# Kernel optimization log

Hardware: AMD Instinct MI355X
Metric: run time of the kernel (lower is better)

The kernel has to match this reference:

```python
import jax, jax.numpy as jnp
import numpy as np

N, E, B = 8000, 128000, 16
DIN, D, H, C, L = 16, 256, 8, 32, 6
MC, NT = 200, 8
NEG_SLOPE = 0.2


def layernorm(x, s, b):
    mu = jnp.mean(x, axis=-1, keepdims=True)
    var = jnp.mean(jnp.square(x - mu), axis=-1, keepdims=True)
    return (x - mu) * jax.lax.rsqrt(var + 1e-5) * s + b


def setup_inputs() -> dict:
    key = jax.random.key(0)
    ks = iter(jax.random.split(key, 64))
    rn = lambda shape, s=0.05: jax.random.normal(next(ks), shape, jnp.float32) * s
    inp = {}
    inp['x'] = jax.random.normal(next(ks), (N, DIN), jnp.float32)
    inp['edge_index'] = jax.random.randint(next(ks), (2, E), 0, N)
    inp['batch'] = jnp.sort(jax.random.randint(next(ks), (N,), 0, B))
    # node encoder: Linear(DIN,D) + LayerNorm
    inp['enc_W'] = rn((DIN, D)); inp['enc_b'] = jnp.zeros((D,), jnp.float32)
    inp['enc_ls'] = jnp.ones((D,), jnp.float32); inp['enc_lb'] = jnp.zeros((D,), jnp.float32)
    # GATv2 layers (stacked): lin_l, lin_r, att, output bias, post LayerNorm
    inp['Wl'] = rn((L, D, D)); inp['bl'] = jnp.zeros((L, D), jnp.float32)
    inp['Wr'] = rn((L, D, D)); inp['br'] = jnp.zeros((L, D), jnp.float32)
    inp['att'] = rn((L, H, C))
    inp['gb'] = jnp.zeros((L, D), jnp.float32)
    inp['gls'] = jnp.ones((L, D), jnp.float32); inp['glb'] = jnp.zeros((L, D), jnp.float32)
    # color head MLP: D -> D -> D//2 -> MC
    inp['cW1'] = rn((D, D)); inp['cb1'] = jnp.zeros((D,), jnp.float32)
    inp['cW2'] = rn((D, D // 2)); inp['cb2'] = jnp.zeros((D // 2,), jnp.float32)
    inp['cW3'] = rn((D // 2, MC)); inp['cb3'] = jnp.zeros((MC,), jnp.float32)
    # chromatic head: 2D -> D -> D//2 -> MC
    inp['chW1'] = rn((2 * D, D)); inp['chb1'] = jnp.zeros((D,), jnp.float32)
    inp['chW2'] = rn((D, D // 2)); inp['chb2'] = jnp.zeros((D // 2,), jnp.float32)
    inp['chW3'] = rn((D // 2, MC)); inp['chb3'] = jnp.zeros((MC,), jnp.float32)
    # type head: 2D -> 128 -> NT
    inp['tW1'] = rn((2 * D, 128)); inp['tb1'] = jnp.zeros((128,), jnp.float32)
    inp['tW2'] = rn((128, NT)); inp['tb2'] = jnp.zeros((NT,), jnp.float32)
    # difficulty head: 2D -> 64 -> 1, sigmoid * 100
    inp['dW1'] = rn((2 * D, 64)); inp['db1'] = jnp.zeros((64,), jnp.float32)
    inp['dW2'] = rn((64, 1)); inp['db2'] = jnp.zeros((1,), jnp.float32)
    return inp


def reference(x, edge_index, batch, enc_W, enc_b, enc_ls, enc_lb,
              Wl, bl, Wr, br, att, gb, gls, glb,
              cW1, cb1, cW2, cb2, cW3, cb3,
              chW1, chb1, chW2, chb2, chW3, chb3,
              tW1, tb1, tW2, tb2, dW1, db1, dW2, db2):
    n = x.shape[0]
    # node encoder (dropout = identity at inference)
    h = jax.nn.relu(layernorm(x @ enc_W + enc_b, enc_ls, enc_lb))
    # add self loops once (same for every layer)
    sl = jnp.arange(n)
    src = jnp.concatenate([edge_index[0], sl])  # message source j
    dst = jnp.concatenate([edge_index[1], sl])  # message target i
    for i in range(L):
        xl = (h @ Wl[i] + bl[i]).reshape(n, H, C)  # source transform
        xr = (h @ Wr[i] + br[i]).reshape(n, H, C)  # target transform
        # GATv2 attention: a^T LeakyReLU(xl_j + xr_i)
        e = jax.nn.leaky_relu(xl[src] + xr[dst], NEG_SLOPE)  # [E+N, H, C]
        logits = jnp.einsum('ehc,hc->eh', e, att[i])          # [E+N, H]
        # segment softmax over destination node (self-loops guarantee denom > 0)
        m = jax.ops.segment_max(logits, dst, num_segments=n)
        m = jnp.where(jnp.isfinite(m), m, 0.0)
        p = jnp.exp(logits - m[dst])
        denom = jax.ops.segment_sum(p, dst, num_segments=n)
        alpha = p / denom[dst]
        out = jax.ops.segment_sum(xl[src] * alpha[:, :, None], dst, num_segments=n)
        out = out.reshape(n, D) + gb[i]
        h_new = jax.nn.elu(layernorm(out, gls[i], glb[i]))
        h = h + h_new if i > 0 else h_new
    # per-node color logits
    z = jax.nn.relu(h @ cW1 + cb1)
    z = jax.nn.relu(z @ cW2 + cb2)
    node_colors = z @ cW3 + cb3
    # global mean/max pooling per graph
    cnt = jax.ops.segment_sum(jnp.ones((n,), h.dtype), batch, num_segments=B)
    mean_p = jax.ops.segment_sum(h, batch, num_segments=B) / jnp.maximum(cnt, 1.0)[:, None]
    max_p = jax.ops.segment_max(h, batch, num_segments=B)
    max_p = jnp.where(jnp.isfinite(max_p), max_p, 0.0)
    g = jnp.concatenate([mean_p, max_p], axis=1)  # [B, 2D]
    zc = jax.nn.relu(g @ chW1 + chb1)
    zc = jax.nn.relu(zc @ chW2 + chb2)
    chromatic_num = zc @ chW3 + chb3
    zt = jax.nn.relu(g @ tW1 + tb1)
    graph_type = zt @ tW2 + tb2
    zd = jax.nn.relu(g @ dW1 + db1)
    difficulty = jax.nn.sigmoid(zd @ dW2 + db2) * 100.0
    return (node_colors, chromatic_num, graph_type, difficulty)
```

## Files before the change

### kernel.cpp

```cpp
#include <hip/hip_runtime.h>
#include <hip/hip_bf16.h>

constexpr int DIN = 16;
constexpr int D   = 256;
constexpr int NH  = 8;
constexpr int NC  = 32;
constexpr int MC  = 200;
constexpr int NT  = 8;
constexpr int BG  = 16;
constexpr int NL  = 6;
constexpr int PS  = 16;
constexpr float NEG = 0.2f;

typedef __attribute__((ext_vector_type(8))) short bfrag;
typedef __attribute__((ext_vector_type(4))) float f32x4;

__device__ inline unsigned short f2bf(float f) {
    unsigned int u = __float_as_uint(f);
    u += 0x7FFFu + ((u >> 16) & 1u);
    return (unsigned short)(u >> 16);
}
__device__ inline float bf2f(unsigned short u) {
    return __uint_as_float((unsigned int)u << 16);
}

__device__ inline float dot_ilp(const float* g, const float* __restrict__ W, int K, int ldw, int t) {
    float a0 = 0.f, a1 = 0.f, a2 = 0.f, a3 = 0.f;
    for (int k = 0; k < K; k += 4) {
        a0 = fmaf(g[k + 0], W[(k + 0) * ldw + t], a0);
        a1 = fmaf(g[k + 1], W[(k + 1) * ldw + t], a1);
        a2 = fmaf(g[k + 2], W[(k + 2) * ldw + t], a2);
        a3 = fmaf(g[k + 3], W[(k + 3) * ldw + t], a3);
    }
    return (a0 + a1) + (a2 + a3);
}


__device__ inline void enc_node(const float* x, const float* W, const float* b, const float* ls,
                                const float* lb, float* h, int n, int lane) {
    int c4 = lane * 4;
    float xs[DIN];
#pragma unroll
    for (int k = 0; k < DIN; k += 4) {
        float4 xv = *(const float4*)&x[n * DIN + k];
        xs[k] = xv.x; xs[k + 1] = xv.y; xs[k + 2] = xv.z; xs[k + 3] = xv.w;
    }
    float4 a = *(const float4*)&b[c4];
#pragma unroll
    for (int k = 0; k < DIN; k++) {
        float4 wv = *(const float4*)&W[k * D + c4];
        a.x = fmaf(xs[k], wv.x, a.x);
        a.y = fmaf(xs[k], wv.y, a.y);
        a.z = fmaf(xs[k], wv.z, a.z);
        a.w = fmaf(xs[k], wv.w, a.w);
    }
    float s = a.x + a.y + a.z + a.w;
#pragma unroll
    for (int msk = 1; msk <= 32; msk <<= 1) s += __shfl_xor(s, msk);
    float mu = s * (1.f / D);
    float4 dv = make_float4(a.x - mu, a.y - mu, a.z - mu, a.w - mu);
    float v2 = dv.x * dv.x + dv.y * dv.y + dv.z * dv.z + dv.w * dv.w;
#pragma unroll
    for (int msk = 1; msk <= 32; msk <<= 1) v2 += __shfl_xor(v2, msk);
    float rstd = rsqrtf(v2 * (1.f / D) + 1e-5f);
    float4 lsv = *(const float4*)&ls[c4];
    float4 lbv = *(const float4*)&lb[c4];
    float4 y = make_float4(fmaxf(dv.x * rstd * lsv.x + lbv.x, 0.f),
                           fmaxf(dv.y * rstd * lsv.y + lbv.y, 0.f),
                           fmaxf(dv.z * rstd * lsv.z + lbv.z, 0.f),
                           fmaxf(dv.w * rstd * lsv.w + lbv.w, 0.f));
    *(float4*)&h[(size_t)n * D + c4] = y;
}

__device__ inline float4 attn_compute(const unsigned short* xl, const unsigned short* xr,
                                      const int* row_ptr, const int* col, const float* att,
                                      const float* gb, const float* gls, const float* glb,
                                      const float* h, int layer, int n, int lane) {
    int c4 = lane * 4;
    ushort4 xr4 = *(const ushort4*)&xr[(size_t)n * D + c4];
    float4 xrv = make_float4(bf2f(xr4.x), bf2f(xr4.y), bf2f(xr4.z), bf2f(xr4.w));
    float4 av  = *(const float4*)&att[c4];
    int beg = row_ptr[n], end = row_ptr[n + 1];
    int deg = end - beg;
    int myc = col[beg + min(lane, deg - 1)];
    float l = 0.f;
    float4 acc = make_float4(0.f, 0.f, 0.f, 0.f);
    auto loadx = [&](int i) -> ushort4 {
        if (i < deg) {
            int s = (i < 64) ? __shfl(myc, i) : col[beg + i];
            return *(const ushort4*)&xl[(size_t)s * D + c4];
        }
        return make_ushort4(0, 0, 0, 0);
    };
    auto step = [&](ushort4 x4) {
        float4 xlv = make_float4(bf2f(x4.x), bf2f(x4.y), bf2f(x4.z), bf2f(x4.w));
        float sx = xlv.x + xrv.x; sx = sx > 0.f ? sx : NEG * sx;
        float sy = xlv.y + xrv.y; sy = sy > 0.f ? sy : NEG * sy;
        float sz = xlv.z + xrv.z; sz = sz > 0.f ? sz : NEG * sz;
        float sw = xlv.w + xrv.w; sw = sw > 0.f ? sw : NEG * sw;
        float z = av.x * sx + av.y * sy + av.z * sz + av.w * sw;
        z += __shfl_xor(z, 1); z += __shfl_xor(z, 2); z += __shfl_xor(z, 4);
        float p = __expf(z);
        l += p;
        acc.x = fmaf(p, xlv.x, acc.x);
        acc.y = fmaf(p, xlv.y, acc.y);
        acc.z = fmaf(p, xlv.z, acc.z);
        acc.w = fmaf(p, xlv.w, acc.w);
    };
    ushort4 b0 = loadx(0), b1 = loadx(1), b2 = loadx(2), b3 = loadx(3);
    int e = 0;
    for (; e + 4 <= deg; e += 4) {
        ushort4 n0 = loadx(e + 4), n1 = loadx(e + 5), n2 = loadx(e + 6), n3 = loadx(e + 7);
        step(b0); step(b1); step(b2); step(b3);
        b0 = n0; b1 = n1; b2 = n2; b3 = n3;
    }
    if (e + 0 < deg) step(b0);
    if (e + 1 < deg) step(b1);
    if (e + 2 < deg) step(b2);
    float4 gbv = *(const float4*)&gb[c4];
    float rl = 1.f / l;
    float4 o = make_float4(acc.x * rl + gbv.x, acc.y * rl + gbv.y,
                           acc.z * rl + gbv.z, acc.w * rl + gbv.w);
    float s = o.x + o.y + o.z + o.w;
#pragma unroll
    for (int msk = 1; msk <= 32; msk <<= 1) s += __shfl_xor(s, msk);
    float mu = s * (1.f / D);
    float4 dv = make_float4(o.x - mu, o.y - mu, o.z - mu, o.w - mu);
    float v2 = dv.x * dv.x + dv.y * dv.y + dv.z * dv.z + dv.w * dv.w;
#pragma unroll
    for (int msk = 1; msk <= 32; msk <<= 1) v2 += __shfl_xor(v2, msk);
    float rstd = rsqrtf(v2 * (1.f / D) + 1e-5f);
    float4 glsv = *(const float4*)&gls[c4];
    float4 glbv = *(const float4*)&glb[c4];
    float y0 = dv.x * rstd * glsv.x + glbv.x;
    float y1 = dv.y * rstd * glsv.y + glbv.y;
    float y2 = dv.z * rstd * glsv.z + glbv.z;
    float y3 = dv.w * rstd * glsv.w + glbv.w;
    y0 = y0 > 0.f ? y0 : expm1f(y0);
    y1 = y1 > 0.f ? y1 : expm1f(y1);
    y2 = y2 > 0.f ? y2 : expm1f(y2);
    y3 = y3 > 0.f ? y3 : expm1f(y3);
    float4 prev = make_float4(0.f, 0.f, 0.f, 0.f);
    if (layer > 0) prev = *(const float4*)&h[(size_t)n * D + c4];
    return make_float4(prev.x + y0, prev.y + y1, prev.z + y2, prev.w + y3);
}

__device__ inline void gemm_one_ct(const unsigned short (*As)[264],
                                   const unsigned short* WpL, const unsigned short* WpR,
                                   const float* bl, const float* br,
                                   unsigned short* xl, unsigned short* xr,
                                   int N, int nb, int ctg, int lane) {
    int m = lane & 15, q = lane >> 4;
    float bLv = bl[ctg * 16 + m];
    float bRv = br[ctg * 16 + m];
    f32x4 accL = (f32x4){bLv, bLv, bLv, bLv};
    f32x4 accR = (f32x4){bRv, bRv, bRv, bRv};
#pragma unroll
    for (int ks = 0; ks < 8; ks++) {
        bfrag af = *(const bfrag*)&As[m][ks * 32 + q * 8];
        size_t off = (((size_t)ctg * 8 + ks) * 64 + lane) * 8;
        bfrag bL = *(const bfrag*)&WpL[off];
        bfrag bR = *(const bfrag*)&WpR[off];
        accL = __builtin_amdgcn_mfma_f32_16x16x32_bf16(af, bL, accL, 0, 0, 0);
        accR = __builtin_amdgcn_mfma_f32_16x16x32_bf16(af, bR, accR, 0, 0, 0);
    }
    int colg = ctg * 16 + m;
#pragma unroll
    for (int reg = 0; reg < 4; reg++) {
        int row = nb + q * 4 + reg;
        if (row < N) {
            xl[(size_t)row * D + colg] = f2bf(accL[reg]);
            xr[(size_t)row * D + colg] = f2bf(accR[reg]);
        }
    }
}

__device__ inline void gemm_core(const unsigned short (*As)[264],
                                 const unsigned short* WpL, const unsigned short* WpR,
                                 const float* bl, const float* br,
                                 unsigned short* xl, unsigned short* xr, int N, int nb, int T) {
    int lane = T & 63, w = T >> 6;
#pragma unroll
    for (int ct = 0; ct < 4; ct++)
        gemm_one_ct(As, WpL, WpR, bl, br, xl, xr, N, nb, w * 4 + ct, lane);
}

__device__ inline void repack_attn_one(const float* Wl, const float* Wr, unsigned short* Wp, int tid) {
    int lane = tid & 63;
    int r1 = tid >> 6;
    int ks = r1 & 7;
    int r2 = r1 >> 3;
    int ct = r2 & 15;
    int mi = r2 >> 4;
    int layer = mi >> 1, mat = mi & 1;
    const float* W = (mat == 0 ? Wl : Wr) + (size_t)layer * D * D;
    int n = ct * 16 + (lane & 15);
    int kb = ks * 32 + (lane >> 4) * 8;
    size_t base = (((size_t)(mi * 16 + ct) * 8 + ks) * 64 + lane) * 8;
#pragma unroll
    for (int j = 0; j < 8; j++) Wp[base + j] = f2bf(W[(size_t)(kb + j) * D + n]);
}

__device__ inline void repack_gen_one(const float* W, unsigned short* Wp, int K, int NCOL, int nks, int tid) {
    int lane = tid & 63;
    int r = tid >> 6;
    int ks = r % nks;
    int ct = r / nks;
    int n = ct * 16 + (lane & 15);
    int kb = ks * 32 + (lane >> 4) * 8;
    size_t base = (((size_t)ct * nks + ks) * 64 + lane) * 8;
#pragma unroll
    for (int j = 0; j < 8; j++) {
        int k = kb + j;
        Wp[base + j] = (n < NCOL && k < K) ? f2bf(W[(size_t)k * NCOL + n]) : (unsigned short)0;
    }
}


__global__ __launch_bounds__(256) void init_enc_k(const float* __restrict__ x, const float* __restrict__ W,
                                                  const float* __restrict__ b, const float* __restrict__ ls,
                                                  const float* __restrict__ lb, float* __restrict__ h,
                                                  int* __restrict__ deg, int N) {
    int gid = blockIdx.x * 256 + threadIdx.x;
    if (gid < N) deg[gid] = 1;
    int lane = threadIdx.x & 63;
    int n = blockIdx.x * 4 + (threadIdx.x >> 6);
    if (n < N) enc_node(x, W, b, ls, lb, h, n, lane);
}

__global__ __launch_bounds__(256) void count_repack_k(const int* __restrict__ dst, int* __restrict__ deg, int E,
                                                      const float* __restrict__ Wl, const float* __restrict__ Wr,
                                                      unsigned short* __restrict__ Wp,
                                                      const float* __restrict__ cW1, unsigned short* __restrict__ cW1p,
                                                      const float* __restrict__ cW2, unsigned short* __restrict__ cW2p,
                                                      const float* __restrict__ cW3, unsigned short* __restrict__ cW3p) {
    int gid = blockIdx.x * 256 + threadIdx.x;
    if (gid < E) atomicAdd(&deg[dst[gid]], 1);
    if (gid < NL * 2 * 16 * 8 * 64) repack_attn_one(Wl, Wr, Wp, gid);
    if (gid < 16 * 8 * 64) repack_gen_one(cW1, cW1p, D, D, 8, gid);
    if (gid < 8 * 8 * 64)  repack_gen_one(cW2, cW2p, D, 128, 8, gid);
    if (gid < 13 * 4 * 64) repack_gen_one(cW3, cW3p, 128, MC, 4, gid);
}

__global__ __launch_bounds__(1024) void scan_k(const int* __restrict__ deg, int* __restrict__ row_ptr,
                                               int* __restrict__ fill, int N) {
    __shared__ int sd[1024];
    int t = threadIdx.x;
    int chunk = (N + 1023) >> 10;
    int lo = t * chunk, hi = min(lo + chunk, N);
    int s = 0;
    for (int i = lo; i < hi; i++) s += deg[i];
    sd[t] = s;
    __syncthreads();
    for (int off = 1; off < 1024; off <<= 1) {
        int v = (t >= off) ? sd[t - off] : 0;
        __syncthreads();
        sd[t] += v;
        __syncthreads();
    }
    int run = (t > 0) ? sd[t - 1] : 0;
    for (int i = lo; i < hi; i++) {
        row_ptr[i] = run; fill[i] = run;
        run += deg[i];
    }
    if (t == 1023) row_ptr[N] = sd[1023];
}

__global__ __launch_bounds__(256) void scatter_gemm0_k(const int* __restrict__ src, const int* __restrict__ dst,
                                                       int* __restrict__ fill, int* __restrict__ col, int E, int N,
                                                       const float* __restrict__ h,
                                                       const unsigned short* __restrict__ WpL,
                                                       const unsigned short* __restrict__ WpR,
                                                       const float* __restrict__ bl, const float* __restrict__ br,
                                                       unsigned short* __restrict__ xl, unsigned short* __restrict__ xr) {
    __shared__ unsigned short As[16][264];
    int T = threadIdx.x;
    int tt = blockIdx.x;
    int ntiles = (N + 15) >> 4;
    if (tt < ntiles) {
        int nb = tt * 16;
#pragma unroll
        for (int r = 0; r < 16; r++) {
            int row = nb + r;
            float v = (row < N) ? h[(size_t)row * D + T] : 0.f;
            As[r][T] = f2bf(v);
        }
        __syncthreads();
        gemm_core(As, WpL, WpR, bl, br, xl, xr, N, nb, T);
    }
    for (int e = blockIdx.x * 256 + T; e < E + N; e += gridDim.x * 256) {
        if (e < E) {
            int p = atomicAdd(&fill[dst[e]], 1);
            col[p] = src[e];
        } else {
            int n = e - E;
            int p = atomicAdd(&fill[n], 1);
            col[p] = n;
        }
    }
}

__global__ __launch_bounds__(256, 8) void attn_k(const unsigned short* __restrict__ xl_in,
                                                 const unsigned short* __restrict__ xr_in,
                                                 const int* __restrict__ row_ptr, const int* __restrict__ col,
                                                 const float* __restrict__ att, const float* __restrict__ gb,
                                                 const float* __restrict__ gls, const float* __restrict__ glb,
                                                 float* __restrict__ h, int layer, int N) {
    int T = threadIdx.x;
    int lane = T & 63, wv = T >> 6;
    int n = blockIdx.x * 4 + wv;
    if (n >= N) return;
    float4 res = attn_compute(xl_in, xr_in, row_ptr, col, att, gb, gls, glb, h, layer, n, lane);
    *(float4*)&h[(size_t)n * D + lane * 4] = res;
}

__global__ __launch_bounds__(256, 4) void gemm_lr_k(const float* __restrict__ h,
                                                    const unsigned short* __restrict__ WpL,
                                                    const unsigned short* __restrict__ WpR,
                                                    const float* __restrict__ bl, const float* __restrict__ br,
                                                    unsigned short* __restrict__ xl, unsigned short* __restrict__ xr,
                                                    int N) {
    __shared__ unsigned short As[16][264];
    int T = threadIdx.x;
    int nb = blockIdx.x * 16;
#pragma unroll
    for (int r = 0; r < 16; r++) {
        int row = nb + r;
        float v = (row < N) ? h[(size_t)row * D + T] : 0.f;
        As[r][T] = f2bf(v);
    }
    __syncthreads();
    gemm_core(As, WpL, WpR, bl, br, xl, xr, N, nb, T);
}

__global__ __launch_bounds__(1024) void colorhead_k(const float* __restrict__ h, int N,
                                                    const unsigned short* __restrict__ W1p, const float* __restrict__ b1,
                                                    const unsigned short* __restrict__ W2p, const float* __restrict__ b2,
                                                    const unsigned short* __restrict__ W3p, const float* __restrict__ b3,
                                                    float* __restrict__ out) {
    __shared__ unsigned short As[16][264];
    __shared__ unsigned short Zs[16][264];
    int T = threadIdx.x;
    int lane = T & 63, wv = T >> 6;
    int nb = blockIdx.x * 16;
    int c4 = lane * 4;
    int n = nb + wv;
    if (n < N) {
        float4 v = *(const float4*)&h[(size_t)n * D + c4];
        As[wv][c4 + 0] = f2bf(v.x);
        As[wv][c4 + 1] = f2bf(v.y);
        As[wv][c4 + 2] = f2bf(v.z);
        As[wv][c4 + 3] = f2bf(v.w);
    } else {
        As[wv][c4 + 0] = 0; As[wv][c4 + 1] = 0; As[wv][c4 + 2] = 0; As[wv][c4 + 3] = 0;
    }
    __syncthreads();
    int m = lane & 15, q = lane >> 4;
    {
        float bv = b1[wv * 16 + m];
        f32x4 acc = (f32x4){bv, bv, bv, bv};
#pragma unroll
        for (int ks = 0; ks < 8; ks++) {
            bfrag af = *(const bfrag*)&As[m][ks * 32 + q * 8];
            bfrag bf = *(const bfrag*)&W1p[(((size_t)wv * 8 + ks) * 64 + lane) * 8];
            acc = __builtin_amdgcn_mfma_f32_16x16x32_bf16(af, bf, acc, 0, 0, 0);
        }
        int colg = wv * 16 + m;
#pragma unroll
        for (int reg = 0; reg < 4; reg++)
            Zs[q * 4 + reg][colg] = f2bf(fmaxf(acc[reg], 0.f));
    }
    __syncthreads();
    if (wv < 8) {
        float bv = b2[wv * 16 + m];
        f32x4 acc = (f32x4){bv, bv, bv, bv};
#pragma unroll
        for (int ks = 0; ks < 8; ks++) {
            bfrag af = *(const bfrag*)&Zs[m][ks * 32 + q * 8];
            bfrag bf = *(const bfrag*)&W2p[(((size_t)wv * 8 + ks) * 64 + lane) * 8];
            acc = __builtin_amdgcn_mfma_f32_16x16x32_bf16(af, bf, acc, 0, 0, 0);
        }
        int colg = wv * 16 + m;
#pragma unroll
        for (int reg = 0; reg < 4; reg++)
            As[q * 4 + reg][colg] = f2bf(fmaxf(acc[reg], 0.f));
    }
    __syncthreads();
    if (wv < 13) {
        int colg = wv * 16 + m;
        float bv = (colg < MC) ? b3[colg] : 0.f;
        f32x4 acc = (f32x4){bv, bv, bv, bv};
#pragma unroll
        for (int ks = 0; ks < 4; ks++) {
            bfrag af = *(const bfrag*)&As[m][ks * 32 + q * 8];
            bfrag bf = *(const bfrag*)&W3p[(((size_t)wv * 4 + ks) * 64 + lane) * 8];
            acc = __builtin_amdgcn_mfma_f32_16x16x32_bf16(af, bf, acc, 0, 0, 0);
        }
#pragma unroll
        for (int reg = 0; reg < 4; reg++) {
            int row = nb + q * 4 + reg;
            if (row < N && colg < MC) out[(size_t)row * MC + colg] = acc[reg];
        }
    }
}

__global__ __launch_bounds__(256) void pool_k(const float* __restrict__ h, const int* __restrict__ batch,
                                              float* __restrict__ psum, float* __restrict__ pmax,
                                              int* __restrict__ cnt, int N) {
    int b = blockIdx.x;
    int sl = blockIdx.y;
    int c = threadIdx.x;
    int lo = 0, hi = N;
    while (lo < hi) { int mid = (lo + hi) >> 1; if (batch[mid] < b) lo = mid + 1; else hi = mid; }
    int s0 = lo;
    lo = 0; hi = N;
    while (lo < hi) { int mid = (lo + hi) >> 1; if (batch[mid] < b + 1) lo = mid + 1; else hi = mid; }
    int s1 = lo;
    int len = s1 - s0;
    int chunk = (len + PS - 1) / PS;
    int n0 = s0 + sl * chunk;
    int n1 = min(n0 + chunk, s1);
    float sum = 0.f, mx = -3.0e38f;
    for (int n = n0; n < n1; n++) {
        float v = h[(size_t)n * D + c];
        sum += v;
        mx = fmaxf(mx, v);
    }
    psum[(size_t)(b * PS + sl) * D + c] = sum;
    pmax[(size_t)(b * PS + sl) * D + c] = mx;
    if (c == 0 && sl == 0) cnt[b] = len;
}

__global__ __launch_bounds__(256) void heads_k(const float* __restrict__ psum, const float* __restrict__ pmax,
                                               const int* __restrict__ cnt,
                                               const float* __restrict__ chW1, const float* __restrict__ chb1,
                                               const float* __restrict__ chW2, const float* __restrict__ chb2,
                                               const float* __restrict__ chW3, const float* __restrict__ chb3,
                                               const float* __restrict__ tW1, const float* __restrict__ tb1,
                                               const float* __restrict__ tW2, const float* __restrict__ tb2,
                                               const float* __restrict__ dW1, const float* __restrict__ db1,
                                               const float* __restrict__ dW2, const float* __restrict__ db2,
                                               float* __restrict__ out_ch, float* __restrict__ out_t,
                                               float* __restrict__ out_d) {
    int b = blockIdx.x, sec = blockIdx.y, t = threadIdx.x;
    __shared__ float g[2 * D];
    __shared__ float z1[D];
    __shared__ float z2[128];
    float sum = 0.f, mx = -3.0e38f;
#pragma unroll
    for (int sl = 0; sl < PS; sl++) {
        sum += psum[(size_t)(b * PS + sl) * D + t];
        mx = fmaxf(mx, pmax[(size_t)(b * PS + sl) * D + t]);
    }
    int cn = cnt[b];
    float c = fmaxf((float)cn, 1.f);
    g[t] = sum / c;
    g[D + t] = (cn > 0) ? mx : 0.f;
    __syncthreads();
    if (sec == 0) {
        z1[t] = fmaxf(chb1[t] + dot_ilp(g, chW1, 2 * D, D, t), 0.f);
        __syncthreads();
        if (t < 128) z2[t] = fmaxf(chb2[t] + dot_ilp(z1, chW2, D, 128, t), 0.f);
        __syncthreads();
        if (t < MC) out_ch[b * MC + t] = chb3[t] + dot_ilp(z2, chW3, 128, MC, t);
    } else if (sec == 1) {
        if (t < 128) z1[t] = fmaxf(tb1[t] + dot_ilp(g, tW1, 2 * D, 128, t), 0.f);
        __syncthreads();
        if (t < NT) out_t[b * NT + t] = tb2[t] + dot_ilp(z1, tW2, 128, NT, t);
    } else {
        if (t < 64) z1[t] = fmaxf(db1[t] + dot_ilp(g, dW1, 2 * D, 64, t), 0.f);
        __syncthreads();
        if (t == 0) {
            float a = db2[0] + dot_ilp(z1, dW2, 64, 1, 0);
            out_d[b] = 100.f / (1.f + __expf(-a));
        }
    }
}

extern "C" void kernel_launch(void* const* d_in, const int* in_sizes, int n_in,
                              void* d_out, int out_size, void* d_ws, size_t ws_size,
                              hipStream_t stream) {
    const float* x     = (const float*)d_in[0];
    const int*   ei    = (const int*)d_in[1];
    const int*   batch = (const int*)d_in[2];
    const float* encW  = (const float*)d_in[3];
    const float* encb  = (const float*)d_in[4];
    const float* encls = (const float*)d_in[5];
    const float* enclb = (const float*)d_in[6];
    const float* Wl    = (const float*)d_in[7];
    const float* bl    = (const float*)d_in[8];
    const float* Wr    = (const float*)d_in[9];
    const float* br    = (const float*)d_in[10];
    const float* att   = (const float*)d_in[11];
    const float* gb    = (const float*)d_in[12];
    const float* gls   = (const float*)d_in[13];
    const float* glb   = (const float*)d_in[14];
    const float* cW1   = (const float*)d_in[15];
    const float* cb1   = (const float*)d_in[16];
    const float* cW2   = (const float*)d_in[17];
    const float* cb2   = (const float*)d_in[18];
    const float* cW3   = (const float*)d_in[19];
    const float* cb3   = (const float*)d_in[20];
    const float* chW1  = (const float*)d_in[21];
    const float* chb1  = (const float*)d_in[22];
    const float* chW2  = (const float*)d_in[23];
    const float* chb2  = (const float*)d_in[24];
    const float* chW3  = (const float*)d_in[25];
    const float* chb3  = (const float*)d_in[26];
    const float* tW1   = (const float*)d_in[27];
    const float* tb1   = (const float*)d_in[28];
    const float* tW2   = (const float*)d_in[29];
    const float* tb2   = (const float*)d_in[30];
    const float* dW1   = (const float*)d_in[31];
    const float* db1   = (const float*)d_in[32];
    const float* dW2   = (const float*)d_in[33];
    const float* db2   = (const float*)d_in[34];

    const int N = in_sizes[0] / DIN;
    const int E = in_sizes[1] / 2;
    const int* esrc = ei;
    const int* edst = ei + E;

    char* p = (char*)d_ws;
    auto carve = [&](size_t bytes) { char* r = p; p += (bytes + 255) & ~(size_t)255; return r; };
    int*            row_ptr = (int*)carve((size_t)(N + 1) * 4);
    int*            fill    = (int*)carve((size_t)N * 4);
    int*            deg     = (int*)carve((size_t)N * 4);
    int*            cnt     = (int*)carve((size_t)BG * 4);
    float*          psum    = (float*)carve((size_t)BG * PS * D * 4);
    float*          pmax    = (float*)carve((size_t)BG * PS * D * 4);
    int*            col     = (int*)carve((size_t)(E + N) * 4);
    unsigned short* Wp      = (unsigned short*)carve((size_t)NL * 2 * 65536 * 2);
    unsigned short* cW1p    = (unsigned short*)carve((size_t)16 * 8 * 64 * 8 * 2);
    unsigned short* cW2p    = (unsigned short*)carve((size_t)8 * 8 * 64 * 8 * 2);
    unsigned short* cW3p    = (unsigned short*)carve((size_t)13 * 4 * 64 * 8 * 2);
    float*          h       = (float*)carve((size_t)N * D * 4);
    unsigned short* xlA     = (unsigned short*)carve((size_t)N * D * 2);
    unsigned short* xrA     = (unsigned short*)carve((size_t)N * D * 2);
    unsigned short* xlB     = (unsigned short*)carve((size_t)N * D * 2);
    unsigned short* xrB     = (unsigned short*)carve((size_t)N * D * 2);
    (void)ws_size; (void)n_in; (void)out_size;

    const int ntiles16 = (N + 15) / 16;
    const int nblk4    = (N + 3) / 4;
    const int sblocks = max(ntiles16, (E + N + 255) / 256);

    init_enc_k<<<(N + 3) / 4, 256, 0, stream>>>(x, encW, encb, encls, enclb, h, deg, N);
    count_repack_k<<<512, 256, 0, stream>>>(edst, deg, E, Wl, Wr, Wp, cW1, cW1p, cW2, cW2p, cW3, cW3p);
    scan_k<<<1, 1024, 0, stream>>>(deg, row_ptr, fill, N);
    scatter_gemm0_k<<<sblocks, 256, 0, stream>>>(esrc, edst, fill, col, E, N, h,
                                                 Wp + 0, Wp + (size_t)65536,
                                                 bl + 0, br + 0, xlA, xrA);
    for (int l = 0; l < NL - 1; l++) {
        const unsigned short* xin_l = (l & 1) ? xlB : xlA;
        const unsigned short* xin_r = (l & 1) ? xrB : xrA;
        unsigned short* xout_l = (l & 1) ? xlA : xlB;
        unsigned short* xout_r = (l & 1) ? xrA : xrB;
        attn_k<<<nblk4, 256, 0, stream>>>(xin_l, xin_r, row_ptr, col, att + l * NH * NC,
                                          gb + l * D, gls + l * D, glb + l * D, h, l, N);
        gemm_lr_k<<<ntiles16, 256, 0, stream>>>(h,
                                                Wp + (size_t)((l + 1) * 2 + 0) * 65536,
                                                Wp + (size_t)((l + 1) * 2 + 1) * 65536,
                                                bl + (l + 1) * D, br + (l + 1) * D, xout_l, xout_r, N);
    }
    float* out = (float*)d_out;
    attn_k<<<nblk4, 256, 0, stream>>>(xlB, xrB, row_ptr, col, att + (NL - 1) * NH * NC,
                                      gb + (NL - 1) * D, gls + (NL - 1) * D, glb + (NL - 1) * D,
                                      h, NL - 1, N);
    colorhead_k<<<ntiles16, 1024, 0, stream>>>(h, N, cW1p, cb1, cW2p, cb2, cW3p, cb3, out);
    pool_k<<<dim3(BG, PS), 256, 0, stream>>>(h, batch, psum, pmax, cnt, N);
    heads_k<<<dim3(BG, 3), 256, 0, stream>>>(psum, pmax, cnt, chW1, chb1, chW2, chb2, chW3, chb3,
                                             tW1, tb1, tW2, tb2, dW1, db1, dW2, db2,
                                             out + (size_t)N * MC,
                                             out + (size_t)N * MC + BG * MC,
                                             out + (size_t)N * MC + BG * MC + BG * NT);
}
```

Baseline: 419.8 us.

## Fuse attention with next-layer GEMM, and fuse init, pooling and heads kernels

Merges each layer's attention kernel with the following lin_l/lin_r GEMM into one 1024-thread block per 16-node tile, so the bf16 A tile comes straight from registers instead of being re-read from h. The last attention layer is fused with the color head, and pooling is fused with the graph heads. Encoder init is merged with degree counting and weight repacking, with the self-loop +1 moved into the scan. This cuts kernel launches and the global round-trips of h, but attention now runs at 16 nodes per block with lower occupancy and gemm_one_ct per wave. Pooling uses only 16 blocks.

```diff
diff --git a/kernel.cpp b/kernel.cpp
--- a/kernel.cpp
+++ b/kernel.cpp
@@ -9,7 +9,6 @@
 constexpr int NT  = 8;
 constexpr int BG  = 16;
 constexpr int NL  = 6;
-constexpr int PS  = 16;
 constexpr float NEG = 0.2f;
 
 typedef __attribute__((ext_vector_type(8))) short bfrag;
@@ -217,24 +216,19 @@
 }
 
 
-__global__ __launch_bounds__(256) void init_enc_k(const float* __restrict__ x, const float* __restrict__ W,
-                                                  const float* __restrict__ b, const float* __restrict__ ls,
-                                                  const float* __restrict__ lb, float* __restrict__ h,
-                                                  int* __restrict__ deg, int N) {
+__global__ __launch_bounds__(256) void fused_init_k(const float* __restrict__ x, const float* __restrict__ encW,
+                                                    const float* __restrict__ encb, const float* __restrict__ encls,
+                                                    const float* __restrict__ enclb, float* __restrict__ h, int N,
+                                                    const int* __restrict__ dst, int* __restrict__ deg, int E,
+                                                    const float* __restrict__ Wl, const float* __restrict__ Wr,
+                                                    unsigned short* __restrict__ Wp,
+                                                    const float* __restrict__ cW1, unsigned short* __restrict__ cW1p,
+                                                    const float* __restrict__ cW2, unsigned short* __restrict__ cW2p,
+                                                    const float* __restrict__ cW3, unsigned short* __restrict__ cW3p) {
     int gid = blockIdx.x * 256 + threadIdx.x;
-    if (gid < N) deg[gid] = 1;
     int lane = threadIdx.x & 63;
     int n = blockIdx.x * 4 + (threadIdx.x >> 6);
-    if (n < N) enc_node(x, W, b, ls, lb, h, n, lane);
-}
-
-__global__ __launch_bounds__(256) void count_repack_k(const int* __restrict__ dst, int* __restrict__ deg, int E,
-                                                      const float* __restrict__ Wl, const float* __restrict__ Wr,
-                                                      unsigned short* __restrict__ Wp,
-                                                      const float* __restrict__ cW1, unsigned short* __restrict__ cW1p,
-                                                      const float* __restrict__ cW2, unsigned short* __restrict__ cW2p,
-                                                      const float* __restrict__ cW3, unsigned short* __restrict__ cW3p) {
-    int gid = blockIdx.x * 256 + threadIdx.x;
+    if (n < N) enc_node(x, encW, encb, encls, enclb, h, n, lane);
     if (gid < E) atomicAdd(&deg[dst[gid]], 1);
     if (gid < NL * 2 * 16 * 8 * 64) repack_attn_one(Wl, Wr, Wp, gid);
     if (gid < 16 * 8 * 64) repack_gen_one(cW1, cW1p, D, D, 8, gid);
@@ -249,7 +243,7 @@
     int chunk = (N + 1023) >> 10;
     int lo = t * chunk, hi = min(lo + chunk, N);
     int s = 0;
-    for (int i = lo; i < hi; i++) s += deg[i];
+    for (int i = lo; i < hi; i++) s += deg[i] + 1;
     sd[t] = s;
     __syncthreads();
     for (int off = 1; off < 1024; off <<= 1) {
@@ -261,7 +255,7 @@
     int run = (t > 0) ? sd[t - 1] : 0;
     for (int i = lo; i < hi; i++) {
         row_ptr[i] = run; fill[i] = run;
-        run += deg[i];
+        run += deg[i] + 1;
     }
     if (t == 1023) row_ptr[N] = sd[1023];
 }
@@ -300,44 +294,46 @@
     }
 }
 
-__global__ __launch_bounds__(256, 8) void attn_k(const unsigned short* __restrict__ xl_in,
-                                                 const unsigned short* __restrict__ xr_in,
-                                                 const int* __restrict__ row_ptr, const int* __restrict__ col,
-                                                 const float* __restrict__ att, const float* __restrict__ gb,
-                                                 const float* __restrict__ gls, const float* __restrict__ glb,
-                                                 float* __restrict__ h, int layer, int N) {
+__global__ __launch_bounds__(1024) void layer_k(const unsigned short* __restrict__ xl_in,
+                                                const unsigned short* __restrict__ xr_in,
+                                                const int* __restrict__ row_ptr, const int* __restrict__ col,
+                                                const float* __restrict__ att, const float* __restrict__ gb,
+                                                const float* __restrict__ gls, const float* __restrict__ glb,
+                                                float* __restrict__ h, int layer, int N,
+                                                const unsigned short* __restrict__ WpL,
+                                                const unsigned short* __restrict__ WpR,
+                                                const float* __restrict__ bl, const float* __restrict__ br,
+                                                unsigned short* __restrict__ xl_out, unsigned short* __restrict__ xr_out) {
+    __shared__ unsigned short As[16][264];
     int T = threadIdx.x;
     int lane = T & 63, wv = T >> 6;
-    int n = blockIdx.x * 4 + wv;
-    if (n >= N) return;
-    float4 res = attn_compute(xl_in, xr_in, row_ptr, col, att, gb, gls, glb, h, layer, n, lane);
-    *(float4*)&h[(size_t)n * D + lane * 4] = res;
-}
-
-__global__ __launch_bounds__(256, 4) void gemm_lr_k(const float* __restrict__ h,
-                                                    const unsigned short* __restrict__ WpL,
-                                                    const unsigned short* __restrict__ WpR,
-                                                    const float* __restrict__ bl, const float* __restrict__ br,
-                                                    unsigned short* __restrict__ xl, unsigned short* __restrict__ xr,
-                                                    int N) {
-    __shared__ unsigned short As[16][264];
-    int T = threadIdx.x;
     int nb = blockIdx.x * 16;
-#pragma unroll
-    for (int r = 0; r < 16; r++) {
-        int row = nb + r;
-        float v = (row < N) ? h[(size_t)row * D + T] : 0.f;
-        As[r][T] = f2bf(v);
-    }
-    __syncthreads();
-    gemm_core(As, WpL, WpR, bl, br, xl, xr, N, nb, T);
-}
-
-__global__ __launch_bounds__(1024) void colorhead_k(const float* __restrict__ h, int N,
-                                                    const unsigned short* __restrict__ W1p, const float* __restrict__ b1,
-                                                    const unsigned short* __restrict__ W2p, const float* __restrict__ b2,
-                                                    const unsigned short* __restrict__ W3p, const float* __restrict__ b3,
-                                                    float* __restrict__ out) {
+    int c4 = lane * 4;
+    int n = nb + wv;
+    if (n < N) {
+        float4 r = attn_compute(xl_in, xr_in, row_ptr, col, att, gb, gls, glb, h, layer, n, lane);
+        *(float4*)&h[(size_t)n * D + c4] = r;
+        As[wv][c4 + 0] = f2bf(r.x);
+        As[wv][c4 + 1] = f2bf(r.y);
+        As[wv][c4 + 2] = f2bf(r.z);
+        As[wv][c4 + 3] = f2bf(r.w);
+    } else {
+        As[wv][c4 + 0] = 0; As[wv][c4 + 1] = 0; As[wv][c4 + 2] = 0; As[wv][c4 + 3] = 0;
+    }
+    __syncthreads();
+    gemm_one_ct((const unsigned short (*)[264])As, WpL, WpR, bl, br, xl_out, xr_out, N, nb, wv, lane);
+}
+
+__global__ __launch_bounds__(1024) void last_k(const unsigned short* __restrict__ xl_in,
+                                               const unsigned short* __restrict__ xr_in,
+                                               const int* __restrict__ row_ptr, const int* __restrict__ col,
+                                               const float* __restrict__ att, const float* __restrict__ gb,
+                                               const float* __restrict__ gls, const float* __restrict__ glb,
+                                               float* __restrict__ h, int N,
+                                               const unsigned short* __restrict__ W1p, const float* __restrict__ b1,
+                                               const unsigned short* __restrict__ W2p, const float* __restrict__ b2,
+                                               const unsigned short* __restrict__ W3p, const float* __restrict__ b3,
+                                               float* __restrict__ out) {
     __shared__ unsigned short As[16][264];
     __shared__ unsigned short Zs[16][264];
     int T = threadIdx.x;
@@ -346,11 +342,12 @@
     int c4 = lane * 4;
     int n = nb + wv;
     if (n < N) {
-        float4 v = *(const float4*)&h[(size_t)n * D + c4];
-        As[wv][c4 + 0] = f2bf(v.x);
-        As[wv][c4 + 1] = f2bf(v.y);
-        As[wv][c4 + 2] = f2bf(v.z);
-        As[wv][c4 + 3] = f2bf(v.w);
+        float4 res = attn_compute(xl_in, xr_in, row_ptr, col, att, gb, gls, glb, h, NL - 1, n, lane);
+        *(float4*)&h[(size_t)n * D + c4] = res;
+        As[wv][c4 + 0] = f2bf(res.x);
+        As[wv][c4 + 1] = f2bf(res.y);
+        As[wv][c4 + 2] = f2bf(res.z);
+        As[wv][c4 + 3] = f2bf(res.w);
     } else {
         As[wv][c4 + 0] = 0; As[wv][c4 + 1] = 0; As[wv][c4 + 2] = 0; As[wv][c4 + 3] = 0;
     }
@@ -404,12 +401,19 @@
     }
 }
 
-__global__ __launch_bounds__(256) void pool_k(const float* __restrict__ h, const int* __restrict__ batch,
-                                              float* __restrict__ psum, float* __restrict__ pmax,
-                                              int* __restrict__ cnt, int N) {
-    int b = blockIdx.x;
-    int sl = blockIdx.y;
-    int c = threadIdx.x;
+__global__ __launch_bounds__(1024) void poolheads_k(const float* __restrict__ h, const int* __restrict__ batch,
+                                                    int N,
+                                                    const float* __restrict__ chW1, const float* __restrict__ chb1,
+                                                    const float* __restrict__ chW2, const float* __restrict__ chb2,
+                                                    const float* __restrict__ chW3, const float* __restrict__ chb3,
+                                                    const float* __restrict__ tW1, const float* __restrict__ tb1,
+                                                    const float* __restrict__ tW2, const float* __restrict__ tb2,
+                                                    const float* __restrict__ dW1, const float* __restrict__ db1,
+                                                    const float* __restrict__ dW2, const float* __restrict__ db2,
+                                                    float* __restrict__ out_ch, float* __restrict__ out_t,
+                                                    float* __restrict__ out_d) {
+    int b = blockIdx.x, t = threadIdx.x;
+    int sl = t >> 8, c = t & 255;
     int lo = 0, hi = N;
     while (lo < hi) { int mid = (lo + hi) >> 1; if (batch[mid] < b) lo = mid + 1; else hi = mid; }
     int s0 = lo;
@@ -417,63 +421,47 @@
     while (lo < hi) { int mid = (lo + hi) >> 1; if (batch[mid] < b + 1) lo = mid + 1; else hi = mid; }
     int s1 = lo;
     int len = s1 - s0;
-    int chunk = (len + PS - 1) / PS;
+    int chunk = (len + 3) >> 2;
     int n0 = s0 + sl * chunk;
     int n1 = min(n0 + chunk, s1);
     float sum = 0.f, mx = -3.0e38f;
-    for (int n = n0; n < n1; n++) {
-        float v = h[(size_t)n * D + c];
-        sum += v;
-        mx = fmaxf(mx, v);
-    }
-    psum[(size_t)(b * PS + sl) * D + c] = sum;
-    pmax[(size_t)(b * PS + sl) * D + c] = mx;
-    if (c == 0 && sl == 0) cnt[b] = len;
-}
-
-__global__ __launch_bounds__(256) void heads_k(const float* __restrict__ psum, const float* __restrict__ pmax,
-                                               const int* __restrict__ cnt,
-                                               const float* __restrict__ chW1, const float* __restrict__ chb1,
-                                               const float* __restrict__ chW2, const float* __restrict__ chb2,
-                                               const float* __restrict__ chW3, const float* __restrict__ chb3,
-                                               const float* __restrict__ tW1, const float* __restrict__ tb1,
-                                               const float* __restrict__ tW2, const float* __restrict__ tb2,
-                                               const float* __restrict__ dW1, const float* __restrict__ db1,
-                                               const float* __restrict__ dW2, const float* __restrict__ db2,
-                                               float* __restrict__ out_ch, float* __restrict__ out_t,
-                                               float* __restrict__ out_d) {
-    int b = blockIdx.x, sec = blockIdx.y, t = threadIdx.x;
+    int n = n0;
+    for (; n + 4 <= n1; n += 4) {
+        float v0 = h[(size_t)(n + 0) * D + c];
+        float v1 = h[(size_t)(n + 1) * D + c];
+        float v2 = h[(size_t)(n + 2) * D + c];
+        float v3 = h[(size_t)(n + 3) * D + c];
+        sum += (v0 + v1) + (v2 + v3);
+        mx = fmaxf(mx, fmaxf(fmaxf(v0, v1), fmaxf(v2, v3)));
+    }
+    for (; n < n1; n++) { float v = h[(size_t)n * D + c]; sum += v; mx = fmaxf(mx, v); }
+    __shared__ float ps[4][256];
+    __shared__ float pm[4][256];
     __shared__ float g[2 * D];
     __shared__ float z1[D];
     __shared__ float z2[128];
-    float sum = 0.f, mx = -3.0e38f;
-#pragma unroll
-    for (int sl = 0; sl < PS; sl++) {
-        sum += psum[(size_t)(b * PS + sl) * D + t];
-        mx = fmaxf(mx, pmax[(size_t)(b * PS + sl) * D + t]);
-    }
-    int cn = cnt[b];
-    float c = fmaxf((float)cn, 1.f);
-    g[t] = sum / c;
-    g[D + t] = (cn > 0) ? mx : 0.f;
-    __syncthreads();
-    if (sec == 0) {
-        z1[t] = fmaxf(chb1[t] + dot_ilp(g, chW1, 2 * D, D, t), 0.f);
-        __syncthreads();
-        if (t < 128) z2[t] = fmaxf(chb2[t] + dot_ilp(z1, chW2, D, 128, t), 0.f);
-        __syncthreads();
-        if (t < MC) out_ch[b * MC + t] = chb3[t] + dot_ilp(z2, chW3, 128, MC, t);
-    } else if (sec == 1) {
-        if (t < 128) z1[t] = fmaxf(tb1[t] + dot_ilp(g, tW1, 2 * D, 128, t), 0.f);
-        __syncthreads();
-        if (t < NT) out_t[b * NT + t] = tb2[t] + dot_ilp(z1, tW2, 128, NT, t);
-    } else {
-        if (t < 64) z1[t] = fmaxf(db1[t] + dot_ilp(g, dW1, 2 * D, 64, t), 0.f);
-        __syncthreads();
-        if (t == 0) {
-            float a = db2[0] + dot_ilp(z1, dW2, 64, 1, 0);
-            out_d[b] = 100.f / (1.f + __expf(-a));
-        }
+    ps[sl][c] = sum; pm[sl][c] = mx;
+    __syncthreads();
+    if (t < 256) {
+        float s = (ps[0][t] + ps[1][t]) + (ps[2][t] + ps[3][t]);
+        float m = fmaxf(fmaxf(pm[0][t], pm[1][t]), fmaxf(pm[2][t], pm[3][t]));
+        g[t] = s / fmaxf((float)len, 1.f);
+        g[D + t] = (len > 0) ? m : 0.f;
+    }
+    __syncthreads();
+    if (t < 256) z1[t] = fmaxf(chb1[t] + dot_ilp(g, chW1, 2 * D, D, t), 0.f);
+    __syncthreads();
+    if (t < 128) z2[t] = fmaxf(chb2[t] + dot_ilp(z1, chW2, D, 128, t), 0.f);
+    __syncthreads();
+    if (t < MC) out_ch[b * MC + t] = chb3[t] + dot_ilp(z2, chW3, 128, MC, t);
+    if (t < 128) z1[t] = fmaxf(tb1[t] + dot_ilp(g, tW1, 2 * D, 128, t), 0.f);
+    __syncthreads();
+    if (t < NT) out_t[b * NT + t] = tb2[t] + dot_ilp(z1, tW2, 128, NT, t);
+    if (t < 64) z2[t] = fmaxf(db1[t] + dot_ilp(g, dW1, 2 * D, 64, t), 0.f);
+    __syncthreads();
+    if (t == 0) {
+        float a = db2[0] + dot_ilp(z2, dW2, 64, 1, 0);
+        out_d[b] = 100.f / (1.f + __expf(-a));
     }
 }
 
@@ -526,9 +514,6 @@
     int*            row_ptr = (int*)carve((size_t)(N + 1) * 4);
     int*            fill    = (int*)carve((size_t)N * 4);
     int*            deg     = (int*)carve((size_t)N * 4);
-    int*            cnt     = (int*)carve((size_t)BG * 4);
-    float*          psum    = (float*)carve((size_t)BG * PS * D * 4);
-    float*          pmax    = (float*)carve((size_t)BG * PS * D * 4);
     int*            col     = (int*)carve((size_t)(E + N) * 4);
     unsigned short* Wp      = (unsigned short*)carve((size_t)NL * 2 * 65536 * 2);
     unsigned short* cW1p    = (unsigned short*)carve((size_t)16 * 8 * 64 * 8 * 2);
@@ -542,11 +527,13 @@
     (void)ws_size; (void)n_in; (void)out_size;
 
     const int ntiles16 = (N + 15) / 16;
-    const int nblk4    = (N + 3) / 4;
-    const int sblocks = max(ntiles16, (E + N + 255) / 256);
-
-    init_enc_k<<<(N + 3) / 4, 256, 0, stream>>>(x, encW, encb, encls, enclb, h, deg, N);
-    count_repack_k<<<512, 256, 0, stream>>>(edst, deg, E, Wl, Wr, Wp, cW1, cW1p, cW2, cW2p, cW3, cW3p);
+    const int sblocks  = max(ntiles16, (E + N + 255) / 256);
+    const int fblocks  = max((N + 3) / 4, max((E + 255) / 256, 384));
+
+    hipMemsetAsync(deg, 0, (size_t)N * 4, stream);
+    fused_init_k<<<fblocks, 256, 0, stream>>>(x, encW, encb, encls, enclb, h, N,
+                                              edst, deg, E, Wl, Wr, Wp,
+                                              cW1, cW1p, cW2, cW2p, cW3, cW3p);
     scan_k<<<1, 1024, 0, stream>>>(deg, row_ptr, fill, N);
     scatter_gemm0_k<<<sblocks, 256, 0, stream>>>(esrc, edst, fill, col, E, N, h,
                                                  Wp + 0, Wp + (size_t)65536,
@@ -556,22 +543,19 @@
         const unsigned short* xin_r = (l & 1) ? xrB : xrA;
         unsigned short* xout_l = (l & 1) ? xlA : xlB;
         unsigned short* xout_r = (l & 1) ? xrA : xrB;
-        attn_k<<<nblk4, 256, 0, stream>>>(xin_l, xin_r, row_ptr, col, att + l * NH * NC,
-                                          gb + l * D, gls + l * D, glb + l * D, h, l, N);
-        gemm_lr_k<<<ntiles16, 256, 0, stream>>>(h,
-                                                Wp + (size_t)((l + 1) * 2 + 0) * 65536,
-                                                Wp + (size_t)((l + 1) * 2 + 1) * 65536,
-                                                bl + (l + 1) * D, br + (l + 1) * D, xout_l, xout_r, N);
+        layer_k<<<ntiles16, 1024, 0, stream>>>(xin_l, xin_r, row_ptr, col, att + l * NH * NC,
+                                               gb + l * D, gls + l * D, glb + l * D, h, l, N,
+                                               Wp + (size_t)((l + 1) * 2 + 0) * 65536,
+                                               Wp + (size_t)((l + 1) * 2 + 1) * 65536,
+                                               bl + (l + 1) * D, br + (l + 1) * D, xout_l, xout_r);
     }
     float* out = (float*)d_out;
-    attn_k<<<nblk4, 256, 0, stream>>>(xlB, xrB, row_ptr, col, att + (NL - 1) * NH * NC,
-                                      gb + (NL - 1) * D, gls + (NL - 1) * D, glb + (NL - 1) * D,
-                                      h, NL - 1, N);
-    colorhead_k<<<ntiles16, 1024, 0, stream>>>(h, N, cW1p, cb1, cW2p, cb2, cW3p, cb3, out);
-    pool_k<<<dim3(BG, PS), 256, 0, stream>>>(h, batch, psum, pmax, cnt, N);
-    heads_k<<<dim3(BG, 3), 256, 0, stream>>>(psum, pmax, cnt, chW1, chb1, chW2, chb2, chW3, chb3,
-                                             tW1, tb1, tW2, tb2, dW1, db1, dW2, db2,
-                                             out + (size_t)N * MC,
-                                             out + (size_t)N * MC + BG * MC,
-                                             out + (size_t)N * MC + BG * MC + BG * NT);
-}
+    last_k<<<ntiles16, 1024, 0, stream>>>(xlB, xrB, row_ptr, col, att + (NL - 1) * NH * NC,
+                                          gb + (NL - 1) * D, gls + (NL - 1) * D, glb + (NL - 1) * D, h, N,
+                                          cW1p, cb1, cW2p, cb2, cW3p, cb3, out);
+    poolheads_k<<<BG, 1024, 0, stream>>>(h, batch, N, chW1, chb1, chW2, chb2, chW3, chb3,
+                                         tW1, tb1, tW2, tb2, dW1, db1, dW2, db2,
+                                         out + (size_t)N * MC,
+                                         out + (size_t)N * MC + BG * MC,
+                                         out + (size_t)N * MC + BG * MC + BG * NT);
+}
```

New measurement: 447.8 us. +6.7%, slower.
